# Optimization experiments

Measured on AMD Instinct MI355X. Metric: run time of the kernel, lower is better.

Reference implementation:

```python
import jax, jax.numpy as jnp
import numpy as np

B = 262144
INPUT_SIZE = 128
HIDDEN_SIZE = 128
EPS = 1e-08


def rms_norm(x, eps=EPS):
    # NB: despite the name, the original subtracts the mean (LayerNorm without affine)
    mean = jnp.mean(x, axis=-1, keepdims=True)
    var = jnp.var(x, axis=-1, keepdims=True)  # biased, matches unbiased=False
    return (x - mean) / jnp.sqrt(var + eps)


def activation_quant(x):
    s = 127.0 / jnp.max(jnp.abs(x), axis=-1, keepdims=True)
    return jnp.clip(jnp.round(s * x), -128.0, 127.0) / s


def matmul_free_linear(x, w_t):
    # w_t is ternary {-1,0,1}, shape [in, out]; original uses two masked matmuls
    pos = (w_t == 1.0).astype(x.dtype)
    neg = (w_t == -1.0).astype(x.dtype)
    return x @ pos - x @ neg


def setup_inputs() -> dict:
    key = jax.random.key(0)
    k1, k2, k3, k4, k5 = jax.random.split(key, 5)
    return {
        "x_t": jax.random.normal(k1, (B, INPUT_SIZE), dtype=jnp.float32),
        "h_t_minus_1": jax.random.normal(k2, (B, HIDDEN_SIZE), dtype=jnp.float32),
        "W_f": jax.random.normal(k3, (HIDDEN_SIZE, INPUT_SIZE), dtype=jnp.float32) * 0.01,
        "W_c": jax.random.normal(k4, (HIDDEN_SIZE, INPUT_SIZE), dtype=jnp.float32) * 0.01,
        "W_g": jax.random.normal(k5, (HIDDEN_SIZE, INPUT_SIZE), dtype=jnp.float32) * 0.01,
        "b_f": jnp.zeros((HIDDEN_SIZE,), dtype=jnp.float32),
        "b_c": jnp.zeros((HIDDEN_SIZE,), dtype=jnp.float32),
        "b_g": jnp.zeros((HIDDEN_SIZE,), dtype=jnp.float32),
    }


def reference(x_t, h_t_minus_1, W_f, W_c, W_g, b_f, b_c, b_g):
    x = activation_quant(rms_norm(x_t, EPS))
    Wf_t = jnp.sign(W_f).T  # [in, hidden]
    Wc_t = jnp.sign(W_c).T
    Wg_t = jnp.sign(W_g).T
    f_t = jax.nn.sigmoid(matmul_free_linear(x, Wf_t) + b_f)
    c_t = jax.nn.silu(matmul_free_linear(x, Wc_t) + b_c)
    g_t = jax.nn.sigmoid(matmul_free_linear(x, Wg_t) + b_g)
    h_t = f_t * h_t_minus_1 + (1.0 - f_t) * c_t
    o_t = g_t * h_t
    return (o_t, h_t)
```

## Files before the change

kernel.cpp:

```cpp
#include <hip/hip_runtime.h>
#include <math.h>

#define WPB 4
#define RG  8

__device__ __forceinline__ int dot4(int a, int b, int c) {
#if defined(__has_builtin)
#if __has_builtin(__builtin_amdgcn_sdot4)
    return __builtin_amdgcn_sdot4(a, b, c, false);
#define DOT4_DONE 1
#endif
#endif
#ifndef DOT4_DONE
    int r = c;
    r += ((a << 24) >> 24) * ((b << 24) >> 24);
    r += ((a << 16) >> 24) * ((b << 16) >> 24);
    r += ((a <<  8) >> 24) * ((b <<  8) >> 24);
    r += ( a        >> 24) * ( b        >> 24);
    return r;
#endif
}

__device__ __forceinline__ float sigmoidf_(float v) {
    return 1.0f / (1.0f + __expf(-v));
}

__global__ __launch_bounds__(256, 3)
void mlgru_kernel(const float* __restrict__ x,
                  const float* __restrict__ hprev,
                  const float* __restrict__ Wf,
                  const float* __restrict__ Wc,
                  const float* __restrict__ Wg,
                  const float* __restrict__ bf,
                  const float* __restrict__ bc,
                  const float* __restrict__ bg,
                  float* __restrict__ out,
                  int nrows)
{
    __shared__ int   wlds[3 * 32 * 128];
    __shared__ short qlds[WPB][RG][64];

    const int tid  = threadIdx.x;
    const int lane = tid & 63;
    const int widx = tid >> 6;

    for (int idx = tid; idx < 3 * 4096; idx += 256) {
        const int g   = idx >> 12;
        const int rem = idx & 4095;
        const int j   = rem >> 5;
        const int w   = rem & 31;
        const float* Wp = (g == 0) ? Wf : ((g == 1) ? Wc : Wg);
        const float4 v = *(const float4*)(Wp + j * 128 + w * 4);
        const int b0 = (v.x > 0.f) - (v.x < 0.f);
        const int b1 = (v.y > 0.f) - (v.y < 0.f);
        const int b2 = (v.z > 0.f) - (v.z < 0.f);
        const int b3 = (v.w > 0.f) - (v.w < 0.f);
        wlds[g * 4096 + w * 128 + j] =
            (b0 & 0xFF) | ((b1 & 0xFF) << 8) | ((b2 & 0xFF) << 16) | ((b3 & 0xFF) << 24);
    }

    const float2 vbf = *(const float2*)(bf + 2 * lane);
    const float2 vbc = *(const float2*)(bc + 2 * lane);
    const float2 vbg = *(const float2*)(bg + 2 * lane);
    __syncthreads();

    const int gw   = blockIdx.x * WPB + widx;
    const int nw   = gridDim.x * WPB;
    const int ngrp = nrows / RG;
    const long long hoff = (long long)nrows * 128;

    for (int grp = gw; grp < ngrp; grp += nw) {
        const int row0 = grp * RG;

        float invs[RG];
        float2 xv[RG];
        #pragma unroll
        for (int r = 0; r < RG; ++r)
            xv[r] = *(const float2*)(x + (long long)(row0 + r) * 128 + 2 * lane);

        #pragma unroll
        for (int r = 0; r < RG; ++r) {
            float s  = xv[r].x + xv[r].y;
            float ss = xv[r].x * xv[r].x + xv[r].y * xv[r].y;
            #pragma unroll
            for (int off = 32; off >= 1; off >>= 1) {
                s  += __shfl_xor(s, off);
                ss += __shfl_xor(ss, off);
            }
            const float mean = s * (1.0f / 128.0f);
            const float var  = ss * (1.0f / 128.0f) - mean * mean;
            const float rstd = rsqrtf(var + 1e-8f);
            const float y0 = (xv[r].x - mean) * rstd;
            const float y1 = (xv[r].y - mean) * rstd;
            float a = fmaxf(fabsf(y0), fabsf(y1));
            #pragma unroll
            for (int off = 32; off >= 1; off >>= 1)
                a = fmaxf(a, __shfl_xor(a, off));
            const float sq = 127.0f / a;
            invs[r] = a * (1.0f / 127.0f);
            int q0 = (int)rintf(y0 * sq);
            int q1 = (int)rintf(y1 * sq);
            q0 = max(-128, min(127, q0));
            q1 = max(-128, min(127, q1));
            qlds[widx][r][lane] = (short)((q0 & 0xFF) | ((q1 & 0xFF) << 8));
        }
        __asm__ __volatile__("s_waitcnt lgkmcnt(0)" ::: "memory");

        int acc[3][2][RG];
        #pragma unroll
        for (int g = 0; g < 3; ++g)
            #pragma unroll
            for (int h = 0; h < 2; ++h)
                #pragma unroll
                for (int r = 0; r < RG; ++r)
                    acc[g][h][r] = 0;

        const int* qrow = (const int*)(&qlds[widx][0][0]);

        #pragma unroll 2
        for (int w4 = 0; w4 < 8; ++w4) {
            int qa[RG][4];
            #pragma unroll
            for (int r = 0; r < RG; ++r) {
                const int4 t = *(const int4*)(qrow + r * 32 + w4 * 4);
                qa[r][0] = t.x; qa[r][1] = t.y; qa[r][2] = t.z; qa[r][3] = t.w;
            }
            #pragma unroll
            for (int wi = 0; wi < 4; ++wi) {
                const int w = w4 * 4 + wi;
                #pragma unroll
                for (int g = 0; g < 3; ++g) {
                    const int2 wv = *(const int2*)(&wlds[g * 4096 + w * 128 + 2 * lane]);
                    #pragma unroll
                    for (int r = 0; r < RG; ++r) {
                        acc[g][0][r] = dot4(qa[r][wi], wv.x, acc[g][0][r]);
                        acc[g][1][r] = dot4(qa[r][wi], wv.y, acc[g][1][r]);
                    }
                }
            }
        }

        #pragma unroll
        for (int r = 0; r < RG; ++r) {
            const long long rbase = (long long)(row0 + r) * 128 + 2 * lane;
            const float2 hp = *(const float2*)(hprev + rbase);
            const float inv = invs[r];

            const float f0 = sigmoidf_((float)acc[0][0][r] * inv + vbf.x);
            const float f1 = sigmoidf_((float)acc[0][1][r] * inv + vbf.y);
            const float cx0 = (float)acc[1][0][r] * inv + vbc.x;
            const float cx1 = (float)acc[1][1][r] * inv + vbc.y;
            const float c0 = cx0 * sigmoidf_(cx0);
            const float c1 = cx1 * sigmoidf_(cx1);
            const float g0 = sigmoidf_((float)acc[2][0][r] * inv + vbg.x);
            const float g1 = sigmoidf_((float)acc[2][1][r] * inv + vbg.y);

            const float h0 = f0 * hp.x + (1.0f - f0) * c0;
            const float h1 = f1 * hp.y + (1.0f - f1) * c1;
            const float o0 = g0 * h0;
            const float o1 = g1 * h1;

            *(float2*)(out + rbase)        = make_float2(o0, o1);
            *(float2*)(out + hoff + rbase) = make_float2(h0, h1);
        }
    }
}

extern "C" void kernel_launch(void* const* d_in, const int* in_sizes, int n_in,
                              void* d_out, int out_size, void* d_ws, size_t ws_size,
                              hipStream_t stream) {
    const float* x  = (const float*)d_in[0];
    const float* h  = (const float*)d_in[1];
    const float* Wf = (const float*)d_in[2];
    const float* Wc = (const float*)d_in[3];
    const float* Wg = (const float*)d_in[4];
    const float* bf = (const float*)d_in[5];
    const float* bc = (const float*)d_in[6];
    const float* bg = (const float*)d_in[7];
    float* out = (float*)d_out;
    const int nrows = in_sizes[0] / 128;

    hipLaunchKernelGGL(mlgru_kernel, dim3(768), dim3(256), 0, stream,
                       x, h, Wf, Wc, Wg, bf, bc, bg, out, nrows);
}
```

Before: 540.3 us.

## Replace sdot4 int8 dot products with MFMA i8 matrix instructions

Replaces the per-lane sdot4 accumulation over 8-row groups with MFMA 16x16x64 int8 instructions over 16-row tiles. Each lane now quantizes a slice of one row, with quad-level shuffles replacing the full-wave reductions and no LDS staging of activations. Ternary weights are stored as padded signed-byte rows in LDS so they can be read as B operands. Block size goes to 512 threads with a 512-block grid. The epilogue writes scalar floats strided across rows, so global stores are less vectorized, which trades store efficiency for much cheaper compute.

```diff
diff --git a/kernel.cpp b/kernel.cpp
--- a/kernel.cpp
+++ b/kernel.cpp
@@ -1,167 +1,153 @@
 #include <hip/hip_runtime.h>
 #include <math.h>
 
-#define WPB 4
-#define RG  8
+typedef int vi4 __attribute__((ext_vector_type(4)));
 
-__device__ __forceinline__ int dot4(int a, int b, int c) {
-#if defined(__has_builtin)
-#if __has_builtin(__builtin_amdgcn_sdot4)
-    return __builtin_amdgcn_sdot4(a, b, c, false);
-#define DOT4_DONE 1
-#endif
-#endif
-#ifndef DOT4_DONE
-    int r = c;
-    r += ((a << 24) >> 24) * ((b << 24) >> 24);
-    r += ((a << 16) >> 24) * ((b << 16) >> 24);
-    r += ((a <<  8) >> 24) * ((b <<  8) >> 24);
-    r += ( a        >> 24) * ( b        >> 24);
-    return r;
-#endif
-}
+#define WAVES   8
+#define THREADS 512
+#define WSTRIDE 144
 
 __device__ __forceinline__ float sigmoidf_(float v) {
     return 1.0f / (1.0f + __expf(-v));
 }
 
-__global__ __launch_bounds__(256, 3)
+__global__ __launch_bounds__(THREADS, 4)
 void mlgru_kernel(const float* __restrict__ x,
                   const float* __restrict__ hprev,
                   const float* __restrict__ Wf,
                   const float* __restrict__ Wc,
                   const float* __restrict__ Wg,
-                  const float* __restrict__ bf,
-                  const float* __restrict__ bc,
-                  const float* __restrict__ bg,
+                  const float* __restrict__ bfp,
+                  const float* __restrict__ bcp,
+                  const float* __restrict__ bgp,
                   float* __restrict__ out,
                   int nrows)
 {
-    __shared__ int   wlds[3 * 32 * 128];
-    __shared__ short qlds[WPB][RG][64];
+    __shared__ signed char wsign[3][128][WSTRIDE];
 
     const int tid  = threadIdx.x;
     const int lane = tid & 63;
     const int widx = tid >> 6;
+    const int m    = lane & 15;
+    const int quad = lane >> 4;
 
-    for (int idx = tid; idx < 3 * 4096; idx += 256) {
+    #pragma unroll
+    for (int it = 0; it < 24; ++it) {
+        const int idx = tid + it * THREADS;
         const int g   = idx >> 12;
-        const int rem = idx & 4095;
-        const int j   = rem >> 5;
-        const int w   = rem & 31;
+        const int j   = (idx >> 5) & 127;
+        const int k4  = idx & 31;
         const float* Wp = (g == 0) ? Wf : ((g == 1) ? Wc : Wg);
-        const float4 v = *(const float4*)(Wp + j * 128 + w * 4);
+        const float4 v = *(const float4*)(Wp + j * 128 + k4 * 4);
         const int b0 = (v.x > 0.f) - (v.x < 0.f);
         const int b1 = (v.y > 0.f) - (v.y < 0.f);
         const int b2 = (v.z > 0.f) - (v.z < 0.f);
         const int b3 = (v.w > 0.f) - (v.w < 0.f);
-        wlds[g * 4096 + w * 128 + j] =
+        *(int*)&wsign[g][j][k4 * 4] =
             (b0 & 0xFF) | ((b1 & 0xFF) << 8) | ((b2 & 0xFF) << 16) | ((b3 & 0xFF) << 24);
     }
 
-    const float2 vbf = *(const float2*)(bf + 2 * lane);
-    const float2 vbc = *(const float2*)(bc + 2 * lane);
-    const float2 vbg = *(const float2*)(bg + 2 * lane);
+    float bfv[8], bcv[8], bgv[8];
+    #pragma unroll
+    for (int ct = 0; ct < 8; ++ct) {
+        bfv[ct] = bfp[ct * 16 + m];
+        bcv[ct] = bcp[ct * 16 + m];
+        bgv[ct] = bgp[ct * 16 + m];
+    }
     __syncthreads();
 
-    const int gw   = blockIdx.x * WPB + widx;
-    const int nw   = gridDim.x * WPB;
-    const int ngrp = nrows / RG;
+    const int gw   = blockIdx.x * WAVES + widx;
+    const int nw   = gridDim.x * WAVES;
+    const int ngrp = nrows >> 4;
     const long long hoff = (long long)nrows * 128;
 
     for (int grp = gw; grp < ngrp; grp += nw) {
-        const int row0 = grp * RG;
+        const int row0 = grp << 4;
 
-        float invs[RG];
-        float2 xv[RG];
+        const float* xp = x + (long long)(row0 + m) * 128 + quad * 16;
+        float4 xa[8];
         #pragma unroll
-        for (int r = 0; r < RG; ++r)
-            xv[r] = *(const float2*)(x + (long long)(row0 + r) * 128 + 2 * lane);
+        for (int i = 0; i < 4; ++i) xa[i]     = *(const float4*)(xp + 4 * i);
+        #pragma unroll
+        for (int i = 0; i < 4; ++i) xa[4 + i] = *(const float4*)(xp + 64 + 4 * i);
+
+        float s = 0.f, ss = 0.f;
+        #pragma unroll
+        for (int i = 0; i < 8; ++i) {
+            s  += (xa[i].x + xa[i].y) + (xa[i].z + xa[i].w);
+            ss += xa[i].x * xa[i].x + xa[i].y * xa[i].y
+                + xa[i].z * xa[i].z + xa[i].w * xa[i].w;
+        }
+        s  += __shfl_xor(s, 16);  s  += __shfl_xor(s, 32);
+        ss += __shfl_xor(ss, 16); ss += __shfl_xor(ss, 32);
+        const float mean = s * (1.0f / 128.0f);
+        const float var  = ss * (1.0f / 128.0f) - mean * mean;
+        const float rstd = rsqrtf(var + 1e-8f);
+
+        float amax = 0.f;
+        #pragma unroll
+        for (int i = 0; i < 8; ++i) {
+            xa[i].x = (xa[i].x - mean) * rstd;
+            xa[i].y = (xa[i].y - mean) * rstd;
+            xa[i].z = (xa[i].z - mean) * rstd;
+            xa[i].w = (xa[i].w - mean) * rstd;
+            amax = fmaxf(amax, fmaxf(fmaxf(fabsf(xa[i].x), fabsf(xa[i].y)),
+                                     fmaxf(fabsf(xa[i].z), fabsf(xa[i].w))));
+        }
+        amax = fmaxf(amax, __shfl_xor(amax, 16));
+        amax = fmaxf(amax, __shfl_xor(amax, 32));
+        const float sq  = 127.0f / amax;
+        const float inv = amax * (1.0f / 127.0f);
+
+        int qw[8];
+        #pragma unroll
+        for (int i = 0; i < 8; ++i) {
+            const float f0 = fminf(fmaxf(rintf(xa[i].x * sq), -128.f), 127.f);
+            const float f1 = fminf(fmaxf(rintf(xa[i].y * sq), -128.f), 127.f);
+            const float f2 = fminf(fmaxf(rintf(xa[i].z * sq), -128.f), 127.f);
+            const float f3 = fminf(fmaxf(rintf(xa[i].w * sq), -128.f), 127.f);
+            qw[i] = ((int)f0 & 0xFF) | (((int)f1 & 0xFF) << 8)
+                  | (((int)f2 & 0xFF) << 16) | (((int)f3 & 0xFF) << 24);
+        }
+        const vi4 a0 = { qw[0], qw[1], qw[2], qw[3] };
+        const vi4 a1 = { qw[4], qw[5], qw[6], qw[7] };
+
+        float invr[4];
+        #pragma unroll
+        for (int r = 0; r < 4; ++r) invr[r] = __shfl(inv, quad * 4 + r);
 
         #pragma unroll
-        for (int r = 0; r < RG; ++r) {
-            float s  = xv[r].x + xv[r].y;
-            float ss = xv[r].x * xv[r].x + xv[r].y * xv[r].y;
+        for (int ct = 0; ct < 8; ++ct) {
+            const int jrow = (ct << 4) + m;
+            const vi4 wf0 = *(const vi4*)&wsign[0][jrow][quad * 16];
+            const vi4 wf1 = *(const vi4*)&wsign[0][jrow][64 + quad * 16];
+            const vi4 wc0 = *(const vi4*)&wsign[1][jrow][quad * 16];
+            const vi4 wc1 = *(const vi4*)&wsign[1][jrow][64 + quad * 16];
+            const vi4 wg0 = *(const vi4*)&wsign[2][jrow][quad * 16];
+            const vi4 wg1 = *(const vi4*)&wsign[2][jrow][64 + quad * 16];
+            const vi4 z = { 0, 0, 0, 0 };
+
+            vi4 accF = __builtin_amdgcn_mfma_i32_16x16x64_i8(a0, wf0, z, 0, 0, 0);
+            accF     = __builtin_amdgcn_mfma_i32_16x16x64_i8(a1, wf1, accF, 0, 0, 0);
+            vi4 accC = __builtin_amdgcn_mfma_i32_16x16x64_i8(a0, wc0, z, 0, 0, 0);
+            accC     = __builtin_amdgcn_mfma_i32_16x16x64_i8(a1, wc1, accC, 0, 0, 0);
+            vi4 accG = __builtin_amdgcn_mfma_i32_16x16x64_i8(a0, wg0, z, 0, 0, 0);
+            accG     = __builtin_amdgcn_mfma_i32_16x16x64_i8(a1, wg1, accG, 0, 0, 0);
+
+            const long long cbase = (long long)(row0 + quad * 4) * 128 + (ct << 4) + m;
             #pragma unroll
-            for (int off = 32; off >= 1; off >>= 1) {
-                s  += __shfl_xor(s, off);
-                ss += __shfl_xor(ss, off);
+            for (int r = 0; r < 4; ++r) {
+                const long long addr = cbase + (long long)r * 128;
+                const float hp = hprev[addr];
+                const float iv = invr[r];
+                const float fv = sigmoidf_((float)accF[r] * iv + bfv[ct]);
+                const float cx = (float)accC[r] * iv + bcv[ct];
+                const float cv = cx * sigmoidf_(cx);
+                const float gv = sigmoidf_((float)accG[r] * iv + bgv[ct]);
+                const float hv = fv * hp + (1.0f - fv) * cv;
+                out[addr]        = gv * hv;
+                out[hoff + addr] = hv;
             }
-            const float mean = s * (1.0f / 128.0f);
-            const float var  = ss * (1.0f / 128.0f) - mean * mean;
-            const float rstd = rsqrtf(var + 1e-8f);
-            const float y0 = (xv[r].x - mean) * rstd;
-            const float y1 = (xv[r].y - mean) * rstd;
-            float a = fmaxf(fabsf(y0), fabsf(y1));
-            #pragma unroll
-            for (int off = 32; off >= 1; off >>= 1)
-                a = fmaxf(a, __shfl_xor(a, off));
-            const float sq = 127.0f / a;
-            invs[r] = a * (1.0f / 127.0f);
-            int q0 = (int)rintf(y0 * sq);
-            int q1 = (int)rintf(y1 * sq);
-            q0 = max(-128, min(127, q0));
-            q1 = max(-128, min(127, q1));
-            qlds[widx][r][lane] = (short)((q0 & 0xFF) | ((q1 & 0xFF) << 8));
-        }
-        __asm__ __volatile__("s_waitcnt lgkmcnt(0)" ::: "memory");
-
-        int acc[3][2][RG];
-        #pragma unroll
-        for (int g = 0; g < 3; ++g)
-            #pragma unroll
-            for (int h = 0; h < 2; ++h)
-                #pragma unroll
-                for (int r = 0; r < RG; ++r)
-                    acc[g][h][r] = 0;
-
-        const int* qrow = (const int*)(&qlds[widx][0][0]);
-
-        #pragma unroll 2
-        for (int w4 = 0; w4 < 8; ++w4) {
-            int qa[RG][4];
-            #pragma unroll
-            for (int r = 0; r < RG; ++r) {
-                const int4 t = *(const int4*)(qrow + r * 32 + w4 * 4);
-                qa[r][0] = t.x; qa[r][1] = t.y; qa[r][2] = t.z; qa[r][3] = t.w;
-            }
-            #pragma unroll
-            for (int wi = 0; wi < 4; ++wi) {
-                const int w = w4 * 4 + wi;
-                #pragma unroll
-                for (int g = 0; g < 3; ++g) {
-                    const int2 wv = *(const int2*)(&wlds[g * 4096 + w * 128 + 2 * lane]);
-                    #pragma unroll
-                    for (int r = 0; r < RG; ++r) {
-                        acc[g][0][r] = dot4(qa[r][wi], wv.x, acc[g][0][r]);
-                        acc[g][1][r] = dot4(qa[r][wi], wv.y, acc[g][1][r]);
-                    }
-                }
-            }
-        }
-
-        #pragma unroll
-        for (int r = 0; r < RG; ++r) {
-            const long long rbase = (long long)(row0 + r) * 128 + 2 * lane;
-            const float2 hp = *(const float2*)(hprev + rbase);
-            const float inv = invs[r];
-
-            const float f0 = sigmoidf_((float)acc[0][0][r] * inv + vbf.x);
-            const float f1 = sigmoidf_((float)acc[0][1][r] * inv + vbf.y);
-            const float cx0 = (float)acc[1][0][r] * inv + vbc.x;
-            const float cx1 = (float)acc[1][1][r] * inv + vbc.y;
-            const float c0 = cx0 * sigmoidf_(cx0);
-            const float c1 = cx1 * sigmoidf_(cx1);
-            const float g0 = sigmoidf_((float)acc[2][0][r] * inv + vbg.x);
-            const float g1 = sigmoidf_((float)acc[2][1][r] * inv + vbg.y);
-
-            const float h0 = f0 * hp.x + (1.0f - f0) * c0;
-            const float h1 = f1 * hp.y + (1.0f - f1) * c1;
-            const float o0 = g0 * h0;
-            const float o1 = g1 * h1;
-
-            *(float2*)(out + rbase)        = make_float2(o0, o1);
-            *(float2*)(out + hoff + rbase) = make_float2(h0, h1);
         }
     }
 }
@@ -180,6 +166,6 @@
     float* out = (float*)d_out;
     const int nrows = in_sizes[0] / 128;
 
-    hipLaunchKernelGGL(mlgru_kernel, dim3(768), dim3(256), 0, stream,
+    hipLaunchKernelGGL(mlgru_kernel, dim3(512), dim3(THREADS), 0, stream,
                        x, h, Wf, Wc, Wg, bf, bc, bg, out, nrows);
 }
```

Result: slower. 575.4 us (+6.5%).
